# Performance work log

Measured on AMD Instinct MI355X. Metric: run time of the kernel, lower is better.

Reference implementation:

```python
import jax, jax.numpy as jnp
import numpy as np

MOMENTUM = 0.9
BN_EPS = 1e-5
NORM_EPS = 1e-12
NUM_CLASSES = 10000
DIM_MLP = 512
NUM_EXPERTS = 3
FEAT_DIM = 256
N = 4096


def _l2norm(x, axis=-1):
    # F.normalize: x / max(||x||, eps)
    n = jnp.sqrt(jnp.sum(x * x, axis=axis, keepdims=True))
    return x / jnp.maximum(n, NORM_EPS)


def setup_inputs() -> dict:
    key = jax.random.key(0)
    ks = jax.random.split(key, 8)
    feat_in = jax.random.normal(ks[0], (N, DIM_MLP * NUM_EXPERTS), dtype=jnp.float32)
    label = jax.random.randint(ks[1], (N,), 0, NUM_CLASSES, dtype=jnp.int32)
    # encoder params
    W1 = jax.random.normal(ks[2], (DIM_MLP * NUM_EXPERTS, DIM_MLP), dtype=jnp.float32) / np.sqrt(DIM_MLP * NUM_EXPERTS)
    b1 = jnp.zeros((DIM_MLP,), dtype=jnp.float32)
    gamma = jnp.ones((DIM_MLP,), dtype=jnp.float32)
    beta = jnp.zeros((DIM_MLP,), dtype=jnp.float32)
    W2 = jax.random.normal(ks[3], (DIM_MLP, FEAT_DIM), dtype=jnp.float32) / np.sqrt(DIM_MLP)
    b2 = jnp.zeros((FEAT_DIM,), dtype=jnp.float32)
    # memory bank buffer: randn then row-normalized (as in __init__)
    memory_pt = _l2norm(jax.random.normal(ks[4], (NUM_CLASSES, FEAT_DIM), dtype=jnp.float32))
    return {"feat_in": feat_in, "label": label, "W1": W1, "b1": b1,
            "gamma": gamma, "beta": beta, "W2": W2, "b2": b2,
            "memory_pt": memory_pt}


def _encoder(feat_in, W1, b1, gamma, beta, W2, b2):
    h = feat_in @ W1 + b1                       # [N, dim_mlp]
    # BatchNorm1d in training mode: batch statistics (biased variance)
    mu = jnp.mean(h, axis=0)
    var = jnp.mean((h - mu) ** 2, axis=0)
    h = (h - mu) * jax.lax.rsqrt(var + BN_EPS) * gamma + beta
    h = jax.nn.relu(h)
    out = h @ W2 + b2                           # [N, 256]
    return _l2norm(out, axis=1)


def _update_memory(memory_pt, feat, label):
    # Strictly sequential per-sample momentum update (order matters for
    # duplicate labels), each touched row renormalized — lax.scan recurrence.
    def step(mem, xy):
        x, y = xy
        pt = MOMENTUM * mem[y] + (1.0 - MOMENTUM) * x
        pt = _l2norm(pt, axis=0)
        return mem.at[y].set(pt), None
    mem, _ = jax.lax.scan(step, memory_pt, (feat, label))
    return mem


def reference(feat_in, label, W1, b1, gamma, beta, W2, b2, memory_pt):
    feat = _encoder(feat_in, W1, b1, gamma, beta, W2, b2)   # [N, 256], unit rows
    # memory_pt.detach(): no grad flows through the memory bank
    mem = _update_memory(jax.lax.stop_gradient(memory_pt),
                         jax.lax.stop_gradient(feat), label)
    mem = jax.lax.stop_gradient(mem)
    sim_logit = jnp.einsum('nc,kc->nk', feat, mem)          # [N, K]
    return sim_logit
```

## Files before the change

### kernel.cpp

```cpp
#include <hip/hip_runtime.h>
#include <stdint.h>

typedef _Float16 f16;
typedef _Float16 f16x2 __attribute__((ext_vector_type(2)));
typedef _Float16 f16x4 __attribute__((ext_vector_type(4)));
typedef _Float16 f16x8 __attribute__((ext_vector_type(8)));
typedef float f32x4 __attribute__((ext_vector_type(4)));

typedef __attribute__((address_space(1))) void gvoid;
typedef __attribute__((address_space(3))) void lvoid;

#define NROWS 4096
#define DIMIN 1536
#define DMLP 512
#define FDIM 256
#define NCLS 10000
#define NPAD 10112

__device__ __forceinline__ void load_lds16(const void* g, void* l) {
    __builtin_amdgcn_global_load_lds((gvoid*)g, (lvoid*)l, 16, 0, 0);
}

__global__ __launch_bounds__(256) void gemm_bt_f16(
    const f16* __restrict__ A, const f16* __restrict__ Bt,
    float* __restrict__ C, const float* __restrict__ bias,
    int K, int ldc, int Nstore)
{
    __shared__ f16 As[128 * 32];
    __shared__ f16 Bs[128 * 32];

    const int tid  = threadIdx.x;
    const int lane = tid & 63;
    const int w    = tid >> 6;
    const int wm   = (w >> 1) * 64;
    const int wn   = (w & 1) * 64;
    const int row0 = blockIdx.x * 128;
    const int col0 = blockIdx.y * 128;
    const int quad = lane >> 4;
    const int r16  = lane & 15;

    f32x4 acc[4][4] = {};

    const int c0 = tid, c1 = tid + 256;
    const int ar0 = c0 >> 2, ag0 = (c0 & 3) * 8;
    const int ar1 = c1 >> 2, ag1 = (c1 & 3) * 8;
    const f16* pa0 = A  + (size_t)(row0 + ar0) * K + ag0;
    const f16* pa1 = A  + (size_t)(row0 + ar1) * K + ag1;
    const f16* pb0 = Bt + (size_t)(col0 + ar0) * K + ag0;
    const f16* pb1 = Bt + (size_t)(col0 + ar1) * K + ag1;

    for (int k0 = 0; k0 < K; k0 += 32) {
        load_lds16(pa0 + k0, &As[c0 * 8]);
        load_lds16(pa1 + k0, &As[c1 * 8]);
        load_lds16(pb0 + k0, &Bs[c0 * 8]);
        load_lds16(pb1 + k0, &Bs[c1 * 8]);
        __syncthreads();

        f16x8 af[4], bq[4];
#pragma unroll
        for (int mi = 0; mi < 4; ++mi)
            af[mi] = *(const f16x8*)&As[(wm + mi * 16 + r16) * 32 + quad * 8];
#pragma unroll
        for (int ni = 0; ni < 4; ++ni)
            bq[ni] = *(const f16x8*)&Bs[(wn + ni * 16 + r16) * 32 + quad * 8];
#pragma unroll
        for (int mi = 0; mi < 4; ++mi)
#pragma unroll
            for (int ni = 0; ni < 4; ++ni)
                acc[mi][ni] = __builtin_amdgcn_mfma_f32_16x16x32_f16(
                    af[mi], bq[ni], acc[mi][ni], 0, 0, 0);
        __syncthreads();
    }

#pragma unroll
    for (int mi = 0; mi < 4; ++mi) {
#pragma unroll
        for (int ni = 0; ni < 4; ++ni) {
            int col = col0 + wn + ni * 16 + r16;
            if (col < Nstore) {
                float bv = bias ? bias[col] : 0.0f;
                int rowb = row0 + wm + mi * 16 + quad * 4;
#pragma unroll
                for (int r = 0; r < 4; ++r)
                    C[(size_t)(rowb + r) * ldc + col] = acc[mi][ni][r] + bv;
            }
        }
    }
}

__global__ void zero_k(float* __restrict__ p, int n) {
    int i = blockIdx.x * 256 + threadIdx.x;
    if (i < n) p[i] = 0.0f;
}

__global__ void f32_to_f16_k(const float* __restrict__ in, f16* __restrict__ out, int n4) {
    int i = blockIdx.x * 256 + threadIdx.x;
    if (i >= n4) return;
    float4 v = *(const float4*)&in[(size_t)i * 4];
    f16x4 o = {(f16)v.x, (f16)v.y, (f16)v.z, (f16)v.w};
    *(f16x4*)&out[(size_t)i * 4] = o;
}

__global__ void transpose_to_f16_k(const float* __restrict__ in, f16* __restrict__ out, int R, int C) {
    int idx = blockIdx.x * 256 + threadIdx.x;
    if (idx >= R * C) return;
    int n = idx / R, k = idx - n * R;
    out[idx] = (f16)in[(size_t)k * C + n];
}

__global__ void bn_stats_k(const float* __restrict__ h, float* __restrict__ sums, float* __restrict__ sqs) {
    int t = threadIdx.x, b = blockIdx.x;
    int c = t * 2;
    float s0 = 0.f, s1 = 0.f, q0 = 0.f, q1 = 0.f;
    for (int r = b; r < NROWS; r += 128) {
        float2 v = *(const float2*)&h[(size_t)r * DMLP + c];
        s0 += v.x; s1 += v.y; q0 += v.x * v.x; q1 += v.y * v.y;
    }
    atomicAdd(&sums[c], s0);
    atomicAdd(&sums[c + 1], s1);
    atomicAdd(&sqs[c], q0);
    atomicAdd(&sqs[c + 1], q1);
}

__global__ void bn_apply_k(const float* __restrict__ h, const float* __restrict__ sums,
                           const float* __restrict__ sqs, const float* __restrict__ gamma,
                           const float* __restrict__ beta, f16* __restrict__ out) {
    int i = blockIdx.x * 256 + threadIdx.x;
    int c = (i & 255) * 2;
    float2 v = *(const float2*)&h[(size_t)i * 2];
    const float inv_n = 1.0f / 4096.0f;
    float mu0 = sums[c] * inv_n, mu1 = sums[c + 1] * inv_n;
    float var0 = fmaxf(sqs[c] * inv_n - mu0 * mu0, 0.0f);
    float var1 = fmaxf(sqs[c + 1] * inv_n - mu1 * mu1, 0.0f);
    float sc0 = rsqrtf(var0 + 1e-5f) * gamma[c];
    float sc1 = rsqrtf(var1 + 1e-5f) * gamma[c + 1];
    float o0 = fmaxf((v.x - mu0) * sc0 + beta[c], 0.0f);
    float o1 = fmaxf((v.y - mu1) * sc1 + beta[c + 1], 0.0f);
    f16x2 o = {(f16)o0, (f16)o1};
    *(f16x2*)&out[(size_t)i * 2] = o;
}

__global__ void l2norm_k(const float* __restrict__ X, float* __restrict__ Y, f16* __restrict__ Yh) {
    int wv = (blockIdx.x * 256 + threadIdx.x) >> 6;
    int lane = threadIdx.x & 63;
    float4 v = *(const float4*)&X[(size_t)wv * FDIM + lane * 4];
    float s = v.x * v.x + v.y * v.y + v.z * v.z + v.w * v.w;
#pragma unroll
    for (int off = 32; off > 0; off >>= 1) s += __shfl_xor(s, off);
    float inv = 1.0f / fmaxf(sqrtf(s), 1e-12f);
    float4 o = {v.x * inv, v.y * inv, v.z * inv, v.w * inv};
    *(float4*)&Y[(size_t)wv * FDIM + lane * 4] = o;
    f16x4 oh = {(f16)o.x, (f16)o.y, (f16)o.z, (f16)o.w};
    *(f16x4*)&Yh[(size_t)wv * FDIM + lane * 4] = oh;
}

__global__ void mem_init_k(const float* __restrict__ mp, f16* __restrict__ memh) {
    int i = blockIdx.x * 256 + threadIdx.x;
    int row = i >> 6, c = (i & 63) * 4;
    f16x4 o = {(f16)0.f, (f16)0.f, (f16)0.f, (f16)0.f};
    if (row < NCLS) {
        float4 v = *(const float4*)&mp[(size_t)row * FDIM + c];
        o = (f16x4){(f16)v.x, (f16)v.y, (f16)v.z, (f16)v.w};
    }
    *(f16x4*)&memh[(size_t)row * FDIM + c] = o;
}

__global__ void chain_k(const int* __restrict__ label, const float* __restrict__ feat,
                        const float* __restrict__ mp, f16* __restrict__ memh) {
    int y = (blockIdx.x * 256 + threadIdx.x) >> 6;
    int lane = threadIdx.x & 63;
    if (y >= NCLS) return;
    float4 m = *(const float4*)&mp[(size_t)y * FDIM + lane * 4];
    bool touched = false;
    for (int g = 0; g < 64; ++g) {
        int lab = label[g * 64 + lane];
        unsigned long long mask = __ballot(lab == y);
        while (mask) {
            int b = __builtin_ctzll(mask);
            mask &= mask - 1;
            int i = g * 64 + b;
            float4 x = *(const float4*)&feat[(size_t)i * FDIM + lane * 4];
            m.x = 0.9f * m.x + 0.1f * x.x;
            m.y = 0.9f * m.y + 0.1f * x.y;
            m.z = 0.9f * m.z + 0.1f * x.z;
            m.w = 0.9f * m.w + 0.1f * x.w;
            float s = m.x * m.x + m.y * m.y + m.z * m.z + m.w * m.w;
#pragma unroll
            for (int off = 32; off > 0; off >>= 1) s += __shfl_xor(s, off);
            float inv = 1.0f / fmaxf(sqrtf(s), 1e-12f);
            m.x *= inv; m.y *= inv; m.z *= inv; m.w *= inv;
            touched = true;
        }
    }
    if (touched) {
        f16x4 o = {(f16)m.x, (f16)m.y, (f16)m.z, (f16)m.w};
        *(f16x4*)&memh[(size_t)y * FDIM + lane * 4] = o;
    }
}

extern "C" void kernel_launch(void* const* d_in, const int* in_sizes, int n_in,
                              void* d_out, int out_size, void* d_ws, size_t ws_size,
                              hipStream_t stream) {
    const float* feat_in = (const float*)d_in[0];
    const int*   label   = (const int*)d_in[1];
    const float* W1      = (const float*)d_in[2];
    const float* b1      = (const float*)d_in[3];
    const float* gamma   = (const float*)d_in[4];
    const float* beta    = (const float*)d_in[5];
    const float* W2      = (const float*)d_in[6];
    const float* b2      = (const float*)d_in[7];
    const float* mp      = (const float*)d_in[8];
    float* out = (float*)d_out;

    char* w = (char*)d_ws;
    f16* A1h   = (f16*)w;   w += (size_t)NROWS * DIMIN * 2;
    f16* W1t   = (f16*)w;   w += (size_t)DMLP * DIMIN * 2;
    f16* W2t   = (f16*)w;   w += (size_t)FDIM * DMLP * 2;
    float* h   = (float*)w; w += (size_t)NROWS * DMLP * 4;
    f16* h2    = (f16*)w;   w += (size_t)NROWS * DMLP * 2;
    float* out2= (float*)w; w += (size_t)NROWS * FDIM * 4;
    float* feat= (float*)w; w += (size_t)NROWS * FDIM * 4;
    f16* feath = (f16*)w;   w += (size_t)NROWS * FDIM * 2;
    f16* memh  = (f16*)w;   w += (size_t)NPAD * FDIM * 2;
    float* sums= (float*)w; w += DMLP * 4;
    float* sqs = (float*)w; w += DMLP * 4;

    zero_k<<<4, 256, 0, stream>>>(sums, 2 * DMLP);
    f32_to_f16_k<<<(NROWS * DIMIN / 4) / 256, 256, 0, stream>>>(feat_in, A1h, NROWS * DIMIN / 4);
    transpose_to_f16_k<<<(DIMIN * DMLP) / 256, 256, 0, stream>>>(W1, W1t, DIMIN, DMLP);
    transpose_to_f16_k<<<(DMLP * FDIM) / 256, 256, 0, stream>>>(W2, W2t, DMLP, FDIM);

    {
        dim3 g(NROWS / 128, DMLP / 128);
        gemm_bt_f16<<<g, 256, 0, stream>>>(A1h, W1t, h, b1, DIMIN, DMLP, DMLP);
    }

    bn_stats_k<<<128, 256, 0, stream>>>(h, sums, sqs);
    bn_apply_k<<<(NROWS * DMLP / 2) / 256, 256, 0, stream>>>(h, sums, sqs, gamma, beta, h2);

    {
        dim3 g(NROWS / 128, FDIM / 128);
        gemm_bt_f16<<<g, 256, 0, stream>>>(h2, W2t, out2, b2, DMLP, FDIM, FDIM);
    }

    l2norm_k<<<NROWS / 4, 256, 0, stream>>>(out2, feat, feath);

    mem_init_k<<<NPAD * 64 / 256, 256, 0, stream>>>(mp, memh);
    chain_k<<<NCLS / 4, 256, 0, stream>>>(label, feat, mp, memh);

    {
        dim3 g(NROWS / 128, NPAD / 128);
        gemm_bt_f16<<<g, 256, 0, stream>>>(feath, memh, out, nullptr, FDIM, NCLS, NCLS);
    }
}
```

Before: 348.9 us.

## Template GEMM with BK=64 swizzled LDS, smaller tiles, fuse memory init into chain

Turns the GEMM into a template with a K-step of 64 and XOR-swizzled LDS slots to cut bank conflicts. The encoder GEMMs use 64x64 tiles so more blocks fill the GPU, while the final similarity GEMM stays at 128x128. BatchNorm scale and shift are precomputed once per channel so the apply kernel does a single vectorised fma plus relu. The separate memory-init kernel is folded into chain_k, which now writes every padded row, removing one launch and one pass over the memory bank.

```diff
diff --git a/kernel.cpp b/kernel.cpp
--- a/kernel.cpp
+++ b/kernel.cpp
@@ -21,61 +21,83 @@
     __builtin_amdgcn_global_load_lds((gvoid*)g, (lvoid*)l, 16, 0, 0);
 }
 
-__global__ __launch_bounds__(256) void gemm_bt_f16(
+template<int TM, int TN>
+__global__ __launch_bounds__(256) void gemm_t(
     const f16* __restrict__ A, const f16* __restrict__ Bt,
     float* __restrict__ C, const float* __restrict__ bias,
     int K, int ldc, int Nstore)
 {
-    __shared__ f16 As[128 * 32];
-    __shared__ f16 Bs[128 * 32];
+    constexpr int BK = 64;
+    constexpr int AM = TM / 32;
+    constexpr int AN = TN / 32;
+    constexpr int CA = TM * 8;
+    constexpr int CB = TN * 8;
+    constexpr int RTOT = (CA + CB) / 256;
+
+    __shared__ f16 As[TM * BK];
+    __shared__ f16 Bs[TN * BK];
 
     const int tid  = threadIdx.x;
     const int lane = tid & 63;
     const int w    = tid >> 6;
-    const int wm   = (w >> 1) * 64;
-    const int wn   = (w & 1) * 64;
-    const int row0 = blockIdx.x * 128;
-    const int col0 = blockIdx.y * 128;
+    const int wm   = (w >> 1) * (TM / 2);
+    const int wn   = (w & 1) * (TN / 2);
+    const int row0 = blockIdx.x * TM;
+    const int col0 = blockIdx.y * TN;
     const int quad = lane >> 4;
     const int r16  = lane & 15;
 
-    f32x4 acc[4][4] = {};
-
-    const int c0 = tid, c1 = tid + 256;
-    const int ar0 = c0 >> 2, ag0 = (c0 & 3) * 8;
-    const int ar1 = c1 >> 2, ag1 = (c1 & 3) * 8;
-    const f16* pa0 = A  + (size_t)(row0 + ar0) * K + ag0;
-    const f16* pa1 = A  + (size_t)(row0 + ar1) * K + ag1;
-    const f16* pb0 = Bt + (size_t)(col0 + ar0) * K + ag0;
-    const f16* pb1 = Bt + (size_t)(col0 + ar1) * K + ag1;
-
-    for (int k0 = 0; k0 < K; k0 += 32) {
-        load_lds16(pa0 + k0, &As[c0 * 8]);
-        load_lds16(pa1 + k0, &As[c1 * 8]);
-        load_lds16(pb0 + k0, &Bs[c0 * 8]);
-        load_lds16(pb1 + k0, &Bs[c1 * 8]);
+    f32x4 acc[AM][AN] = {};
+
+    const f16* gsrc[RTOT];
+    f16* ldst[RTOT];
+#pragma unroll
+    for (int r = 0; r < RTOT; ++r) {
+        int c = tid + r * 256;
+        bool isA = (c < CA);
+        int cc = isA ? c : c - CA;
+        int row = cc >> 3;
+        int gs = (cc & 7) ^ (row & 7);
+        gsrc[r] = (isA ? A + (size_t)(row0 + row) * K
+                       : Bt + (size_t)(col0 + row) * K) + gs * 8;
+        ldst[r] = (isA ? As : Bs) + cc * 8;
+    }
+
+    for (int k0 = 0; k0 < K; k0 += BK) {
+#pragma unroll
+        for (int r = 0; r < RTOT; ++r)
+            load_lds16(gsrc[r] + k0, ldst[r]);
         __syncthreads();
 
-        f16x8 af[4], bq[4];
-#pragma unroll
-        for (int mi = 0; mi < 4; ++mi)
-            af[mi] = *(const f16x8*)&As[(wm + mi * 16 + r16) * 32 + quad * 8];
-#pragma unroll
-        for (int ni = 0; ni < 4; ++ni)
-            bq[ni] = *(const f16x8*)&Bs[(wn + ni * 16 + r16) * 32 + quad * 8];
-#pragma unroll
-        for (int mi = 0; mi < 4; ++mi)
-#pragma unroll
-            for (int ni = 0; ni < 4; ++ni)
-                acc[mi][ni] = __builtin_amdgcn_mfma_f32_16x16x32_f16(
-                    af[mi], bq[ni], acc[mi][ni], 0, 0, 0);
+#pragma unroll
+        for (int ks = 0; ks < 2; ++ks) {
+            f16x8 af[AM], bq[AN];
+#pragma unroll
+            for (int mi = 0; mi < AM; ++mi) {
+                int row = wm + mi * 16 + r16;
+                int slot = (ks * 4 + quad) ^ (r16 & 7);
+                af[mi] = *(const f16x8*)&As[row * BK + slot * 8];
+            }
+#pragma unroll
+            for (int ni = 0; ni < AN; ++ni) {
+                int row = wn + ni * 16 + r16;
+                int slot = (ks * 4 + quad) ^ (r16 & 7);
+                bq[ni] = *(const f16x8*)&Bs[row * BK + slot * 8];
+            }
+#pragma unroll
+            for (int mi = 0; mi < AM; ++mi)
+#pragma unroll
+                for (int ni = 0; ni < AN; ++ni)
+                    acc[mi][ni] = __builtin_amdgcn_mfma_f32_16x16x32_f16(
+                        af[mi], bq[ni], acc[mi][ni], 0, 0, 0);
+        }
         __syncthreads();
     }
 
 #pragma unroll
-    for (int mi = 0; mi < 4; ++mi) {
-#pragma unroll
-        for (int ni = 0; ni < 4; ++ni) {
+    for (int mi = 0; mi < AM; ++mi) {
+#pragma unroll
+        for (int ni = 0; ni < AN; ++ni) {
             int col = col0 + wn + ni * 16 + r16;
             if (col < Nstore) {
                 float bv = bias ? bias[col] : 0.0f;
@@ -122,22 +144,31 @@
     atomicAdd(&sqs[c + 1], q1);
 }
 
-__global__ void bn_apply_k(const float* __restrict__ h, const float* __restrict__ sums,
-                           const float* __restrict__ sqs, const float* __restrict__ gamma,
-                           const float* __restrict__ beta, f16* __restrict__ out) {
+__global__ void bn_finish_k(const float* __restrict__ sums, const float* __restrict__ sqs,
+                            const float* __restrict__ gamma, const float* __restrict__ beta,
+                            float* __restrict__ scale, float* __restrict__ shift) {
+    int c = blockIdx.x * 256 + threadIdx.x;
+    if (c >= DMLP) return;
+    const float inv_n = 1.0f / 4096.0f;
+    float mu = sums[c] * inv_n;
+    float var = fmaxf(sqs[c] * inv_n - mu * mu, 0.0f);
+    float a = rsqrtf(var + 1e-5f) * gamma[c];
+    scale[c] = a;
+    shift[c] = beta[c] - mu * a;
+}
+
+__global__ void bn_apply_k(const float* __restrict__ h, const float* __restrict__ scale,
+                           const float* __restrict__ shift, f16* __restrict__ out) {
     int i = blockIdx.x * 256 + threadIdx.x;
-    int c = (i & 255) * 2;
-    float2 v = *(const float2*)&h[(size_t)i * 2];
-    const float inv_n = 1.0f / 4096.0f;
-    float mu0 = sums[c] * inv_n, mu1 = sums[c + 1] * inv_n;
-    float var0 = fmaxf(sqs[c] * inv_n - mu0 * mu0, 0.0f);
-    float var1 = fmaxf(sqs[c + 1] * inv_n - mu1 * mu1, 0.0f);
-    float sc0 = rsqrtf(var0 + 1e-5f) * gamma[c];
-    float sc1 = rsqrtf(var1 + 1e-5f) * gamma[c + 1];
-    float o0 = fmaxf((v.x - mu0) * sc0 + beta[c], 0.0f);
-    float o1 = fmaxf((v.y - mu1) * sc1 + beta[c + 1], 0.0f);
-    f16x2 o = {(f16)o0, (f16)o1};
-    *(f16x2*)&out[(size_t)i * 2] = o;
+    int c = (i & 127) * 4;
+    float4 v = *(const float4*)&h[(size_t)i * 4];
+    float4 sc = *(const float4*)&scale[c];
+    float4 sh = *(const float4*)&shift[c];
+    f16x4 o = {(f16)fmaxf(v.x * sc.x + sh.x, 0.0f),
+               (f16)fmaxf(v.y * sc.y + sh.y, 0.0f),
+               (f16)fmaxf(v.z * sc.z + sh.z, 0.0f),
+               (f16)fmaxf(v.w * sc.w + sh.w, 0.0f)};
+    *(f16x4*)&out[(size_t)i * 4] = o;
 }
 
 __global__ void l2norm_k(const float* __restrict__ X, float* __restrict__ Y, f16* __restrict__ Yh) {
@@ -154,48 +185,35 @@
     *(f16x4*)&Yh[(size_t)wv * FDIM + lane * 4] = oh;
 }
 
-__global__ void mem_init_k(const float* __restrict__ mp, f16* __restrict__ memh) {
-    int i = blockIdx.x * 256 + threadIdx.x;
-    int row = i >> 6, c = (i & 63) * 4;
-    f16x4 o = {(f16)0.f, (f16)0.f, (f16)0.f, (f16)0.f};
-    if (row < NCLS) {
-        float4 v = *(const float4*)&mp[(size_t)row * FDIM + c];
-        o = (f16x4){(f16)v.x, (f16)v.y, (f16)v.z, (f16)v.w};
-    }
-    *(f16x4*)&memh[(size_t)row * FDIM + c] = o;
-}
-
 __global__ void chain_k(const int* __restrict__ label, const float* __restrict__ feat,
                         const float* __restrict__ mp, f16* __restrict__ memh) {
     int y = (blockIdx.x * 256 + threadIdx.x) >> 6;
     int lane = threadIdx.x & 63;
-    if (y >= NCLS) return;
-    float4 m = *(const float4*)&mp[(size_t)y * FDIM + lane * 4];
-    bool touched = false;
-    for (int g = 0; g < 64; ++g) {
-        int lab = label[g * 64 + lane];
-        unsigned long long mask = __ballot(lab == y);
-        while (mask) {
-            int b = __builtin_ctzll(mask);
-            mask &= mask - 1;
-            int i = g * 64 + b;
-            float4 x = *(const float4*)&feat[(size_t)i * FDIM + lane * 4];
-            m.x = 0.9f * m.x + 0.1f * x.x;
-            m.y = 0.9f * m.y + 0.1f * x.y;
-            m.z = 0.9f * m.z + 0.1f * x.z;
-            m.w = 0.9f * m.w + 0.1f * x.w;
-            float s = m.x * m.x + m.y * m.y + m.z * m.z + m.w * m.w;
-#pragma unroll
-            for (int off = 32; off > 0; off >>= 1) s += __shfl_xor(s, off);
-            float inv = 1.0f / fmaxf(sqrtf(s), 1e-12f);
-            m.x *= inv; m.y *= inv; m.z *= inv; m.w *= inv;
-            touched = true;
+    float4 m = {0.f, 0.f, 0.f, 0.f};
+    if (y < NCLS) {
+        m = *(const float4*)&mp[(size_t)y * FDIM + lane * 4];
+        for (int g = 0; g < 64; ++g) {
+            int lab = label[g * 64 + lane];
+            unsigned long long mask = __ballot(lab == y);
+            while (mask) {
+                int b = __builtin_ctzll(mask);
+                mask &= mask - 1;
+                int i = g * 64 + b;
+                float4 x = *(const float4*)&feat[(size_t)i * FDIM + lane * 4];
+                m.x = 0.9f * m.x + 0.1f * x.x;
+                m.y = 0.9f * m.y + 0.1f * x.y;
+                m.z = 0.9f * m.z + 0.1f * x.z;
+                m.w = 0.9f * m.w + 0.1f * x.w;
+                float s = m.x * m.x + m.y * m.y + m.z * m.z + m.w * m.w;
+#pragma unroll
+                for (int off = 32; off > 0; off >>= 1) s += __shfl_xor(s, off);
+                float inv = 1.0f / fmaxf(sqrtf(s), 1e-12f);
+                m.x *= inv; m.y *= inv; m.z *= inv; m.w *= inv;
+            }
         }
     }
-    if (touched) {
-        f16x4 o = {(f16)m.x, (f16)m.y, (f16)m.z, (f16)m.w};
-        *(f16x4*)&memh[(size_t)y * FDIM + lane * 4] = o;
-    }
+    f16x4 o = {(f16)m.x, (f16)m.y, (f16)m.z, (f16)m.w};
+    *(f16x4*)&memh[(size_t)y * FDIM + lane * 4] = o;
 }
 
 extern "C" void kernel_launch(void* const* d_in, const int* in_sizes, int n_in,
@@ -224,6 +242,8 @@
     f16* memh  = (f16*)w;   w += (size_t)NPAD * FDIM * 2;
     float* sums= (float*)w; w += DMLP * 4;
     float* sqs = (float*)w; w += DMLP * 4;
+    float* bnsc= (float*)w; w += DMLP * 4;
+    float* bnsh= (float*)w; w += DMLP * 4;
 
     zero_k<<<4, 256, 0, stream>>>(sums, 2 * DMLP);
     f32_to_f16_k<<<(NROWS * DIMIN / 4) / 256, 256, 0, stream>>>(feat_in, A1h, NROWS * DIMIN / 4);
@@ -231,25 +251,25 @@
     transpose_to_f16_k<<<(DMLP * FDIM) / 256, 256, 0, stream>>>(W2, W2t, DMLP, FDIM);
 
     {
-        dim3 g(NROWS / 128, DMLP / 128);
-        gemm_bt_f16<<<g, 256, 0, stream>>>(A1h, W1t, h, b1, DIMIN, DMLP, DMLP);
+        dim3 g(NROWS / 64, DMLP / 64);
+        gemm_t<64, 64><<<g, 256, 0, stream>>>(A1h, W1t, h, b1, DIMIN, DMLP, DMLP);
     }
 
     bn_stats_k<<<128, 256, 0, stream>>>(h, sums, sqs);
-    bn_apply_k<<<(NROWS * DMLP / 2) / 256, 256, 0, stream>>>(h, sums, sqs, gamma, beta, h2);
+    bn_finish_k<<<2, 256, 0, stream>>>(sums, sqs, gamma, beta, bnsc, bnsh);
+    bn_apply_k<<<(NROWS * DMLP / 4) / 256, 256, 0, stream>>>(h, bnsc, bnsh, h2);
 
     {
-        dim3 g(NROWS / 128, FDIM / 128);
-        gemm_bt_f16<<<g, 256, 0, stream>>>(h2, W2t, out2, b2, DMLP, FDIM, FDIM);
+        dim3 g(NROWS / 64, FDIM / 64);
+        gemm_t<64, 64><<<g, 256, 0, stream>>>(h2, W2t, out2, b2, DMLP, FDIM, FDIM);
     }
 
     l2norm_k<<<NROWS / 4, 256, 0, stream>>>(out2, feat, feath);
 
-    mem_init_k<<<NPAD * 64 / 256, 256, 0, stream>>>(mp, memh);
-    chain_k<<<NCLS / 4, 256, 0, stream>>>(label, feat, mp, memh);
+    chain_k<<<NPAD / 4, 256, 0, stream>>>(label, feat, mp, memh);
 
     {
         dim3 g(NROWS / 128, NPAD / 128);
-        gemm_bt_f16<<<g, 256, 0, stream>>>(feath, memh, out, nullptr, FDIM, NCLS, NCLS);
-    }
-}
+        gemm_t<128, 128><<<g, 256, 0, stream>>>(feath, memh, out, nullptr, FDIM, NCLS, NCLS);
+    }
+}
```

Result: faster. 322.8 us (-7.5%).
